# Kernel tuning notes

Hardware: AMD Instinct MI355X
Metric: run time of the kernel (lower is better)

## Reference

```python
import jax, jax.numpy as jnp
import numpy as np

NUM_CHUNKS = 8
TOP_K = 2
IN_FEATURES = 4096
OUT_FEATURES = 4096
CIN = IN_FEATURES // NUM_CHUNKS    # 512
COUT = OUT_FEATURES // NUM_CHUNKS  # 512
BATCH = 8192


def setup_inputs() -> dict:
    key = jax.random.key(0)
    kx, kw, kb = jax.random.split(key, 3)
    x = jax.random.normal(kx, (BATCH, IN_FEATURES), dtype=jnp.float32)
    # per-chunk Linear params: W[i] is [out_chunk, in_chunk] like nn.Linear.weight
    bound = 1.0 / np.sqrt(CIN)
    W = jax.random.uniform(kw, (NUM_CHUNKS, COUT, CIN), jnp.float32, -bound, bound)
    b = jax.random.uniform(kb, (NUM_CHUNKS, COUT), jnp.float32, -bound, bound)
    return {"x": x, "W": W, "b": b}


def reference(x, W, b):
    B = x.shape[0]
    nc, cout, cin = W.shape
    # split into equal chunks along feature dim: [B, nc, cin]
    xr = x.reshape(B, nc, cin)
    # per-chunk activity: mean |x| over batch and chunk features -> [nc]
    activities = jnp.mean(jnp.abs(xr), axis=(0, 2))
    # select top-k most active chunks (indices are constants w.r.t. grads)
    _, idx = jax.lax.top_k(activities, TOP_K)  # [k]
    xs = xr[:, idx, :]                          # [B, k, cin]
    # grouped GEMM only on selected chunks: y = x @ W^T + b
    ys = jnp.einsum('bki,koi->bko', xs, W[idx]) + b[idx][None]  # [B, k, cout]
    out = jnp.zeros((B, nc, cout), dtype=x.dtype).at[:, idx, :].set(ys)
    return out.reshape(B, nc * cout), activities
```

## Files before the change

kernel.cpp:

```cpp
#include <hip/hip_runtime.h>
#include <hip/hip_bf16.h>

#define BATCH 8192
#define NCH 8
#define CIN 512
#define COUT 512
#define NF 4096

typedef __attribute__((ext_vector_type(8))) __bf16 bf16x8;
typedef __attribute__((ext_vector_type(4))) float f32x4;

__device__ __forceinline__ void async_load16(const void* g, void* l) {
    __builtin_amdgcn_global_load_lds((const __attribute__((address_space(1))) void*)g,
                                     (__attribute__((address_space(3))) void*)l, 16, 0, 0);
}

__device__ __forceinline__ bf16x8 cvt8(const float4 a, const float4 b) {
    bf16x8 p;
    p[0] = (__bf16)a.x; p[1] = (__bf16)a.y; p[2] = (__bf16)a.z; p[3] = (__bf16)a.w;
    p[4] = (__bf16)b.x; p[5] = (__bf16)b.y; p[6] = (__bf16)b.z; p[7] = (__bf16)b.w;
    return p;
}

__global__ __launch_bounds__(256) void prep_kernel(const float* __restrict__ x,
                                                   const float* __restrict__ W,
                                                   __bf16* __restrict__ xbf,
                                                   __bf16* __restrict__ wbf,
                                                   float* __restrict__ sums) {
    const int c = blockIdx.y;
    const int bx = blockIdx.x;
    const int t = threadIdx.x;

    if (bx >= 256) {
        const int q = bx - 256;
        const float* src = W + (size_t)c * (COUT * CIN) + q * 32768;
        __bf16* dst = wbf + (size_t)c * (COUT * CIN) + q * 32768;
#pragma unroll
        for (int p = 0; p < 16; ++p) {
            const int off = p * 2048 + t * 8;
            const float4 a0 = *(const float4*)(src + off);
            const float4 a1 = *(const float4*)(src + off + 4);
            *(bf16x8*)(dst + off) = cvt8(a0, a1);
        }
        return;
    }

    const int rsub = t >> 6;
    const int col = (t & 63) * 8;
    const size_t rbase = (size_t)bx * 32;
    __bf16* xc = xbf + (size_t)c * BATCH * CIN;
    float s = 0.f;
#pragma unroll
    for (int p = 0; p < 8; ++p) {
        const size_t r = rbase + p * 4 + rsub;
        const float* src = x + r * NF + c * CIN + col;
        const float4 a0 = *(const float4*)(src);
        const float4 a1 = *(const float4*)(src + 4);
        s += fabsf(a0.x) + fabsf(a0.y) + fabsf(a0.z) + fabsf(a0.w)
           + fabsf(a1.x) + fabsf(a1.y) + fabsf(a1.z) + fabsf(a1.w);
        *(bf16x8*)(xc + r * CIN + col) = cvt8(a0, a1);
    }
#pragma unroll
    for (int off = 32; off > 0; off >>= 1) s += __shfl_down(s, off, 64);
    __shared__ float red[4];
    const int lane = t & 63, wv = t >> 6;
    if (lane == 0) red[wv] = s;
    __syncthreads();
    if (t == 0) atomicAdd(&sums[c], red[0] + red[1] + red[2] + red[3]);
}

__global__ void topk_kernel(const float* __restrict__ sums,
                            float* __restrict__ out_act,
                            int* __restrict__ idx_out) {
    if (threadIdx.x == 0) {
        const float scale = 1.0f / ((float)BATCH * (float)CIN);
        float a[NCH];
        for (int i = 0; i < NCH; ++i) { a[i] = sums[i] * scale; out_act[i] = a[i]; }
        int i0 = 0;
        for (int i = 1; i < NCH; ++i) if (a[i] > a[i0]) i0 = i;
        int i1 = (i0 == 0) ? 1 : 0;
        for (int i = 0; i < NCH; ++i) if (i != i0 && a[i] > a[i1]) i1 = i;
        idx_out[0] = i0; idx_out[1] = i1;
    }
}

__global__ __launch_bounds__(256) void gemm_kernel(const __bf16* __restrict__ xbf,
                                                   const __bf16* __restrict__ wbf,
                                                   const float* __restrict__ bias,
                                                   const int* __restrict__ idx,
                                                   float* __restrict__ out) {
    const int c = blockIdx.z;
    const int t = threadIdx.x;
    const size_t obase = (size_t)(blockIdx.x * 128) * NF + c * COUT + blockIdx.y * 128;

    if (c != idx[0] && c != idx[1]) {
        const float4 z = make_float4(0.f, 0.f, 0.f, 0.f);
        const int rq = t >> 5;
        const int cq = (t & 31) << 2;
#pragma unroll
        for (int p = 0; p < 16; ++p)
            *(float4*)(out + obase + (size_t)(p * 8 + rq) * NF + cq) = z;
        return;
    }

    __shared__ __bf16 Xs[128 * 32];
    __shared__ __bf16 Wsh[128 * 32];

    const int lane = t & 63, w = t >> 6;
    const int wm = (w >> 1) * 64, wn = (w & 1) * 64;
    const int lr = lane & 15, lq = lane >> 4;

    const int srow = lane >> 2;
    const int skcol = (lane & 3) * 8;
    const __bf16* xg = xbf + (size_t)c * BATCH * CIN
                     + (size_t)(blockIdx.x * 128 + w * 32 + srow) * CIN + skcol;
    const __bf16* wg = wbf + (size_t)c * COUT * CIN
                     + (size_t)(blockIdx.y * 128 + w * 32 + srow) * CIN + skcol;
    __bf16* xls = &Xs[(w * 32) * 32];
    __bf16* wls = &Wsh[(w * 32) * 32];

    f32x4 acc[4][4];
#pragma unroll
    for (int i = 0; i < 4; ++i)
#pragma unroll
        for (int j = 0; j < 4; ++j) acc[i][j] = (f32x4){0.f, 0.f, 0.f, 0.f};

    for (int kk = 0; kk < CIN; kk += 32) {
        async_load16(xg + kk, xls);
        async_load16(xg + kk + (size_t)16 * CIN, xls + 16 * 32);
        async_load16(wg + kk, wls);
        async_load16(wg + kk + (size_t)16 * CIN, wls + 16 * 32);
        __syncthreads();

        bf16x8 av[4], bv[4];
#pragma unroll
        for (int mt = 0; mt < 4; ++mt) av[mt] = *(const bf16x8*)&Xs[(wm + mt * 16 + lr) * 32 + lq * 8];
#pragma unroll
        for (int nt = 0; nt < 4; ++nt) bv[nt] = *(const bf16x8*)&Wsh[(wn + nt * 16 + lr) * 32 + lq * 8];
#pragma unroll
        for (int mt = 0; mt < 4; ++mt)
#pragma unroll
            for (int nt = 0; nt < 4; ++nt)
                acc[mt][nt] = __builtin_amdgcn_mfma_f32_16x16x32_bf16(av[mt], bv[nt], acc[mt][nt], 0, 0, 0);
        __syncthreads();
    }

    float bvv[4];
#pragma unroll
    for (int nt = 0; nt < 4; ++nt)
        bvv[nt] = bias[c * COUT + blockIdx.y * 128 + wn + nt * 16 + lr];
#pragma unroll
    for (int mt = 0; mt < 4; ++mt)
#pragma unroll
        for (int nt = 0; nt < 4; ++nt)
#pragma unroll
            for (int r = 0; r < 4; ++r) {
                const int row = wm + mt * 16 + lq * 4 + r;
                const int col = wn + nt * 16 + lr;
                out[obase + (size_t)row * NF + col] = acc[mt][nt][r] + bvv[nt];
            }
}

extern "C" void kernel_launch(void* const* d_in, const int* in_sizes, int n_in,
                              void* d_out, int out_size, void* d_ws, size_t ws_size,
                              hipStream_t stream) {
    const float* x = (const float*)d_in[0];
    const float* W = (const float*)d_in[1];
    const float* b = (const float*)d_in[2];
    float* out = (float*)d_out;

    float* sums = (float*)d_ws;
    int* idx = (int*)((char*)d_ws + 32);
    __bf16* xbf = (__bf16*)((char*)d_ws + 256);
    __bf16* wbf = (__bf16*)((char*)d_ws + 256 + (size_t)BATCH * NF * 2);

    hipMemsetAsync(d_ws, 0, 64, stream);
    prep_kernel<<<dim3(264, NCH), 256, 0, stream>>>(x, W, xbf, wbf, sums);
    topk_kernel<<<1, 64, 0, stream>>>(sums, out + (size_t)BATCH * NF, idx);
    gemm_kernel<<<dim3(64, 4, NCH), 256, 0, stream>>>(xbf, wbf, b, idx, out);
}
```

Before: 275.6 us.

## Convert only top-k selected chunks to bf16 and fuse top-k into reduction

The activity reduction now runs as a standalone read-only pass, and the last block to finish (found with an atomic counter) computes the top-k, which removes the separate top-k kernel launch. A new conversion kernel then casts only the two selected chunks of x and W to bf16 into compact buffers, instead of converting all eight. The trade is that x's selected chunks are read twice, once in the reduction and once in the conversion, while far fewer bf16 bytes are written. It also adds one extra kernel launch and a last-block-done synchronisation pattern.

```diff
diff --git a/kernel.cpp b/kernel.cpp
--- a/kernel.cpp
+++ b/kernel.cpp
@@ -22,19 +22,68 @@
     return p;
 }
 
-__global__ __launch_bounds__(256) void prep_kernel(const float* __restrict__ x,
-                                                   const float* __restrict__ W,
-                                                   __bf16* __restrict__ xbf,
-                                                   __bf16* __restrict__ wbf,
-                                                   float* __restrict__ sums) {
+__global__ __launch_bounds__(256) void act_kernel(const float* __restrict__ x,
+                                                  float* __restrict__ sums,
+                                                  unsigned int* __restrict__ counter,
+                                                  float* __restrict__ out_act,
+                                                  int* __restrict__ idx_out) {
     const int c = blockIdx.y;
     const int bx = blockIdx.x;
     const int t = threadIdx.x;
+    const int wv = t >> 6;
+    const int col = (t & 63) * 8;
+    const size_t rbase = (size_t)bx * 32;
+    float s = 0.f;
+#pragma unroll
+    for (int p = 0; p < 8; ++p) {
+        const size_t r = rbase + p * 4 + wv;
+        const float* src = x + r * NF + c * CIN + col;
+        const float4 a0 = *(const float4*)(src);
+        const float4 a1 = *(const float4*)(src + 4);
+        s += fabsf(a0.x) + fabsf(a0.y) + fabsf(a0.z) + fabsf(a0.w)
+           + fabsf(a1.x) + fabsf(a1.y) + fabsf(a1.z) + fabsf(a1.w);
+    }
+#pragma unroll
+    for (int off = 32; off > 0; off >>= 1) s += __shfl_down(s, off, 64);
+    __shared__ float red[4];
+    const int lane = t & 63;
+    if (lane == 0) red[wv] = s;
+    __syncthreads();
+    if (t == 0) {
+        atomicAdd(&sums[c], red[0] + red[1] + red[2] + red[3]);
+        __threadfence();
+        const unsigned int old = atomicAdd(counter, 1u);
+        if (old == 256u * NCH - 1u) {
+            __threadfence();
+            const float scale = 1.0f / ((float)BATCH * (float)CIN);
+            float a[NCH];
+            for (int i = 0; i < NCH; ++i) {
+                a[i] = atomicAdd(&sums[i], 0.0f) * scale;
+                out_act[i] = a[i];
+            }
+            int i0 = 0;
+            for (int i = 1; i < NCH; ++i) if (a[i] > a[i0]) i0 = i;
+            int i1 = (i0 == 0) ? 1 : 0;
+            for (int i = 0; i < NCH; ++i) if (i != i0 && a[i] > a[i1]) i1 = i;
+            idx_out[0] = i0; idx_out[1] = i1;
+        }
+    }
+}
+
+__global__ __launch_bounds__(256) void cvt_kernel(const float* __restrict__ x,
+                                                  const float* __restrict__ W,
+                                                  const int* __restrict__ idx,
+                                                  __bf16* __restrict__ xc,
+                                                  __bf16* __restrict__ wc) {
+    const int z = blockIdx.y;
+    const int c = idx[z];
+    const int bx = blockIdx.x;
+    const int t = threadIdx.x;
 
     if (bx >= 256) {
         const int q = bx - 256;
         const float* src = W + (size_t)c * (COUT * CIN) + q * 32768;
-        __bf16* dst = wbf + (size_t)c * (COUT * CIN) + q * 32768;
+        __bf16* dst = wc + (size_t)z * (COUT * CIN) + q * 32768;
 #pragma unroll
         for (int p = 0; p < 16; ++p) {
             const int off = p * 2048 + t * 8;
@@ -45,55 +94,31 @@
         return;
     }
 
-    const int rsub = t >> 6;
+    const int wv = t >> 6;
     const int col = (t & 63) * 8;
     const size_t rbase = (size_t)bx * 32;
-    __bf16* xc = xbf + (size_t)c * BATCH * CIN;
-    float s = 0.f;
+    __bf16* dst = xc + (size_t)z * BATCH * CIN;
 #pragma unroll
     for (int p = 0; p < 8; ++p) {
-        const size_t r = rbase + p * 4 + rsub;
+        const size_t r = rbase + p * 4 + wv;
         const float* src = x + r * NF + c * CIN + col;
         const float4 a0 = *(const float4*)(src);
         const float4 a1 = *(const float4*)(src + 4);
-        s += fabsf(a0.x) + fabsf(a0.y) + fabsf(a0.z) + fabsf(a0.w)
-           + fabsf(a1.x) + fabsf(a1.y) + fabsf(a1.z) + fabsf(a1.w);
-        *(bf16x8*)(xc + r * CIN + col) = cvt8(a0, a1);
-    }
-#pragma unroll
-    for (int off = 32; off > 0; off >>= 1) s += __shfl_down(s, off, 64);
-    __shared__ float red[4];
-    const int lane = t & 63, wv = t >> 6;
-    if (lane == 0) red[wv] = s;
-    __syncthreads();
-    if (t == 0) atomicAdd(&sums[c], red[0] + red[1] + red[2] + red[3]);
-}
-
-__global__ void topk_kernel(const float* __restrict__ sums,
-                            float* __restrict__ out_act,
-                            int* __restrict__ idx_out) {
-    if (threadIdx.x == 0) {
-        const float scale = 1.0f / ((float)BATCH * (float)CIN);
-        float a[NCH];
-        for (int i = 0; i < NCH; ++i) { a[i] = sums[i] * scale; out_act[i] = a[i]; }
-        int i0 = 0;
-        for (int i = 1; i < NCH; ++i) if (a[i] > a[i0]) i0 = i;
-        int i1 = (i0 == 0) ? 1 : 0;
-        for (int i = 0; i < NCH; ++i) if (i != i0 && a[i] > a[i1]) i1 = i;
-        idx_out[0] = i0; idx_out[1] = i1;
-    }
-}
-
-__global__ __launch_bounds__(256) void gemm_kernel(const __bf16* __restrict__ xbf,
-                                                   const __bf16* __restrict__ wbf,
+        *(bf16x8*)(dst + r * CIN + col) = cvt8(a0, a1);
+    }
+}
+
+__global__ __launch_bounds__(256) void gemm_kernel(const __bf16* __restrict__ xc,
+                                                   const __bf16* __restrict__ wc,
                                                    const float* __restrict__ bias,
                                                    const int* __restrict__ idx,
                                                    float* __restrict__ out) {
     const int c = blockIdx.z;
     const int t = threadIdx.x;
     const size_t obase = (size_t)(blockIdx.x * 128) * NF + c * COUT + blockIdx.y * 128;
-
-    if (c != idx[0] && c != idx[1]) {
+    const int i0 = idx[0], i1 = idx[1];
+
+    if (c != i0 && c != i1) {
         const float4 z = make_float4(0.f, 0.f, 0.f, 0.f);
         const int rq = t >> 5;
         const int cq = (t & 31) << 2;
@@ -102,6 +127,7 @@
             *(float4*)(out + obase + (size_t)(p * 8 + rq) * NF + cq) = z;
         return;
     }
+    const int kz = (c == i0) ? 0 : 1;
 
     __shared__ __bf16 Xs[128 * 32];
     __shared__ __bf16 Wsh[128 * 32];
@@ -112,9 +138,9 @@
 
     const int srow = lane >> 2;
     const int skcol = (lane & 3) * 8;
-    const __bf16* xg = xbf + (size_t)c * BATCH * CIN
+    const __bf16* xg = xc + (size_t)kz * BATCH * CIN
                      + (size_t)(blockIdx.x * 128 + w * 32 + srow) * CIN + skcol;
-    const __bf16* wg = wbf + (size_t)c * COUT * CIN
+    const __bf16* wg = wc + (size_t)kz * COUT * CIN
                      + (size_t)(blockIdx.y * 128 + w * 32 + srow) * CIN + skcol;
     __bf16* xls = &Xs[(w * 32) * 32];
     __bf16* wls = &Wsh[(w * 32) * 32];
@@ -170,12 +196,14 @@
     float* out = (float*)d_out;
 
     float* sums = (float*)d_ws;
-    int* idx = (int*)((char*)d_ws + 32);
-    __bf16* xbf = (__bf16*)((char*)d_ws + 256);
-    __bf16* wbf = (__bf16*)((char*)d_ws + 256 + (size_t)BATCH * NF * 2);
+    unsigned int* counter = (unsigned int*)((char*)d_ws + 32);
+    int* idx = (int*)((char*)d_ws + 40);
+    __bf16* xc = (__bf16*)((char*)d_ws + 256);
+    __bf16* wc = (__bf16*)((char*)d_ws + 256 + (size_t)2 * BATCH * CIN * 2);
 
     hipMemsetAsync(d_ws, 0, 64, stream);
-    prep_kernel<<<dim3(264, NCH), 256, 0, stream>>>(x, W, xbf, wbf, sums);
-    topk_kernel<<<1, 64, 0, stream>>>(sums, out + (size_t)BATCH * NF, idx);
-    gemm_kernel<<<dim3(64, 4, NCH), 256, 0, stream>>>(xbf, wbf, b, idx, out);
-}
+    act_kernel<<<dim3(256, NCH), 256, 0, stream>>>(x, sums, counter,
+                                                   out + (size_t)BATCH * NF, idx);
+    cvt_kernel<<<dim3(264, 2), 256, 0, stream>>>(x, W, idx, xc, wc);
+    gemm_kernel<<<dim3(64, 4, NCH), 256, 0, stream>>>(xc, wc, b, idx, out);
+}
```

New measurement: 372.5 us. +35.2%, slower.
